# Kernel tuning notes

Hardware: AMD Instinct MI355X
Metric: run time of the kernel (lower is better)

## Reference

```python
import jax, jax.numpy as jnp
import numpy as np

LN_EPS = 1e-5
SM_EPS = 1e-16  # torch_geometric softmax denominator eps


def _layernorm(x, g, b):
    mu = jnp.mean(x, axis=-1, keepdims=True)
    var = jnp.var(x, axis=-1, keepdims=True)
    return (x - mu) * jax.lax.rsqrt(var + LN_EPS) * g + b


def setup_inputs() -> dict:
    d = 128
    L = 3
    N = 50000
    E = 800000
    key = jax.random.key(0)
    ks = jax.random.split(key, 16)
    s = 1.0 / np.sqrt(d)
    inp = {
        "edge_index": jax.random.randint(ks[0], (2, E), 0, N, dtype=jnp.int32),
        "x": jax.random.normal(ks[1], (N, d), dtype=jnp.float32),
        # per-layer attention params, stacked over layers
        "Wq": jax.random.uniform(ks[2], (L, d, d), jnp.float32, -s, s),
        "bq": jax.random.uniform(ks[3], (L, d), jnp.float32, -s, s),
        "Wk": jax.random.uniform(ks[4], (L, d, d), jnp.float32, -s, s),
        "bk": jax.random.uniform(ks[5], (L, d), jnp.float32, -s, s),
        "Wv": jax.random.uniform(ks[6], (L, d, d), jnp.float32, -s, s),
        "bv": jax.random.uniform(ks[7], (L, d), jnp.float32, -s, s),
        "ln_g": jnp.ones((L, d), jnp.float32),
        "ln_b": jnp.zeros((L, d), jnp.float32),
        # MLP stack: d -> 4d -> 2d -> d (no activations, per source)
        "W1": jax.random.uniform(ks[8], (4 * d, d), jnp.float32, -s, s),
        "b1": jax.random.uniform(ks[9], (4 * d,), jnp.float32, -s, s),
        "W2": jax.random.uniform(ks[10], (2 * d, 4 * d), jnp.float32, -0.5 * s, 0.5 * s),
        "b2": jax.random.uniform(ks[11], (2 * d,), jnp.float32, -0.5 * s, 0.5 * s),
        "W3": jax.random.uniform(ks[12], (d, 2 * d), jnp.float32, -0.7 * s, 0.7 * s),
        "b3": jax.random.uniform(ks[13], (d,), jnp.float32, -0.7 * s, 0.7 * s),
        "Wvec": jax.random.uniform(ks[14], (1, d), jnp.float32, -s, s),
        "bvec": jax.random.uniform(ks[15], (1,), jnp.float32, -s, s),
        "fn_g": jnp.ones((d,), jnp.float32),
        "fn_b": jnp.zeros((d,), jnp.float32),
    }
    return inp


def reference(edge_index, x, Wq, bq, Wk, bk, Wv, bv, ln_g, ln_b,
              W1, b1, W2, b2, W3, b3, Wvec, bvec, fn_g, fn_b):
    N = x.shape[0]
    src = edge_index[0]
    dst = edge_index[1]
    x_i = x[src]  # [E, d]
    x_j = x[dst]  # [E, d]
    L = Wq.shape[0]
    attn_output = None
    query = None
    for i in range(L):
        q = x_i @ Wq[i].T + bq[i]
        k = x_j @ Wk[i].T + bk[i]
        v = x_j @ Wv[i].T + bv[i]
        alpha = jnp.sum(q * k, axis=-1)  # [E]
        # segment softmax over destination node (torch_geometric.utils.softmax)
        m = jax.ops.segment_max(alpha, dst, num_segments=N)
        e = jnp.exp(alpha - m[dst])
        s = jax.ops.segment_sum(e, dst, num_segments=N)
        alpha = e / (s[dst] + SM_EPS)
        attn_output = jax.nn.relu(alpha[:, None] * v)  # dropout = identity (eval)
        query = _layernorm(x_j + attn_output, ln_g[i], ln_b[i])
    adj = attn_output  # squeeze(0) is a no-op for [E, d]
    adj = adj @ W1.T + b1
    adj = adj @ W2.T + b2
    adj = adj @ W3.T + b3
    adj = _layernorm(adj + query, fn_g, fn_b)
    adj_logits = (adj @ Wvec.T + bvec)[:, 0]  # [E]
    return adj_logits
```

## Files before the change

### kernel.cpp

```cpp
#include <hip/hip_runtime.h>


typedef __attribute__((ext_vector_type(8))) short bf16x8;
typedef __attribute__((ext_vector_type(4))) float f32x4;

__device__ __forceinline__ unsigned short f2bf(float f) {
  unsigned int u = __float_as_uint(f);
  unsigned int r = (u + 0x7fffu + ((u >> 16) & 1u)) >> 16;
  return (unsigned short)r;
}
__device__ __forceinline__ float blo(unsigned int u) {
  return __uint_as_float(u << 16);
}
__device__ __forceinline__ float bhi(unsigned int u) {
  return __uint_as_float(u & 0xffff0000u);
}

__global__ __launch_bounds__(128) void k_TW(
    const float* __restrict__ W2, const float* __restrict__ W1,
    const float* __restrict__ Wq, const float* __restrict__ Wk,
    const float* __restrict__ Wv, float* __restrict__ T,
    unsigned short* __restrict__ Wqb, unsigned short* __restrict__ Wkb,
    unsigned short* __restrict__ Wvb, float* __restrict__ sArr, int N) {
  const int b = blockIdx.x, t = threadIdx.x;
  if (b < 256) {
    float acc = 0.f;
    for (int k = 0; k < 512; ++k) acc += W2[b * 512 + k] * W1[k * 128 + t];
    T[b * 128 + t] = acc;
  } else if (b < 640) {
    const int idx = (b - 256) * 128 + t;
    const int m = idx >> 14, i = idx & 16383;
    const float* s = (m == 0) ? Wq : (m == 1) ? Wk : Wv;
    unsigned short* d = (m == 0) ? Wqb : (m == 1) ? Wkb : Wvb;
    d[i] = f2bf(s[i]);
  } else {
    const int i = (b - 640) * 128 + t;
    if (i < N) sArr[i] = 0.f;
  }
}

__global__ __launch_bounds__(256) void k_Ac(
    const float* __restrict__ W3, const float* __restrict__ T,
    const float* __restrict__ W2, const float* __restrict__ b1,
    const float* __restrict__ b2, const float* __restrict__ b3,
    const float* __restrict__ g, const float* __restrict__ lb,
    const float* __restrict__ fg, const float* __restrict__ fb,
    const float* __restrict__ wv, unsigned short* __restrict__ A3b,
    float* __restrict__ cfull, float* __restrict__ C) {
  __shared__ float t1[256];
  __shared__ float cf[128];
  const int b = blockIdx.x, t = threadIdx.x;
  if (b < 64) {
    const int i = 2 * b + (t >> 7), j = t & 127;
    float acc = 0.f;
    for (int k = 0; k < 256; ++k) acc += W3[i * 256 + k] * T[k * 128 + j];
    A3b[i * 128 + j] = f2bf(acc);
    return;
  }
  float acc = b2[t];
  for (int c = 0; c < 512; ++c) acc += W2[t * 512 + c] * b1[c];
  t1[t] = acc;
  __syncthreads();
  if (t < 128) {
    float a = b3[t];
    for (int k = 0; k < 256; ++k) a += W3[t * 256 + k] * t1[k];
    cfull[t] = a;
    cf[t] = a;
  }
  __syncthreads();
  if (t < 64) {
    const int l = t;
    const float2 gv = ((const float2*)g)[l];
    const float2 bv = ((const float2*)lb)[l];
    const float2 fgv = ((const float2*)fg)[l];
    const float2 fbv = ((const float2*)fb)[l];
    const float2 wvv = ((const float2*)wv)[l];
    const float P0 = cf[2 * l] + bv.x, P1 = cf[2 * l + 1] + bv.y;
    const float w0 = fgv.x * wvv.x, w1 = fgv.y * wvv.y;
    float s[9];
    s[0] = P0 + P1;
    s[1] = P0 * w0 + P1 * w1;
    s[2] = P0 * P0 + P1 * P1;
    s[3] = gv.x + gv.y;
    s[4] = gv.x * w0 + gv.y * w1;
    s[5] = gv.x * gv.x + gv.y * gv.y;
    s[6] = P0 * gv.x + P1 * gv.y;
    s[7] = w0 + w1;
    s[8] = fbv.x * wvv.x + fbv.y * wvv.y;
#pragma unroll
    for (int m = 32; m >= 1; m >>= 1)
#pragma unroll
      for (int i = 0; i < 9; ++i) s[i] += __shfl_xor(s[i], m, 64);
    if (l == 0)
#pragma unroll
      for (int i = 0; i < 9; ++i) C[i] = s[i];
  }
}

__global__ __launch_bounds__(256) void k_node(
    const float* __restrict__ x, const unsigned short* __restrict__ Wqb,
    const unsigned short* __restrict__ Wkb,
    const unsigned short* __restrict__ Wvb,
    const unsigned short* __restrict__ A3b, const float* __restrict__ bq,
    const float* __restrict__ bk, const float* __restrict__ bv,
    const float* __restrict__ cfull, const float* __restrict__ g,
    const float* __restrict__ lb, const float* __restrict__ fg,
    const float* __restrict__ wvp, unsigned short* __restrict__ Qb,
    unsigned short* __restrict__ Kb, float* __restrict__ S, int N) {
  __shared__ unsigned short tile[64][136];
  __shared__ unsigned short wl[128 * 128];
  const int t = threadIdx.x;
  const int nb = blockIdx.x * 64;
  for (int i = t; i < 64 * 32; i += 256) {
    const int j = i >> 5, c4 = i & 31;
    const int n = nb + j;
    float4 v = make_float4(0.f, 0.f, 0.f, 0.f);
    if (n < N) v = ((const float4*)x)[(size_t)n * 32 + c4];
    unsigned int lo = f2bf(v.x) | ((unsigned int)f2bf(v.y) << 16);
    unsigned int hi = f2bf(v.z) | ((unsigned int)f2bf(v.w) << 16);
    *(uint2*)&tile[j][c4 << 2] = make_uint2(lo, hi);
  }
  __syncthreads();
  const int wv16 = __builtin_amdgcn_readfirstlane(t >> 6) * 16;
  const int l = t & 63;
  const int ln = l & 15, g4 = l >> 4;
  bf16x8 af[4];
#pragma unroll
  for (int kb = 0; kb < 4; ++kb)
    af[kb] = *(const bf16x8*)&tile[wv16 + ln][kb * 32 + g4 * 8];

#define STAGE_W(MAT)                                                          \
  {                                                                           \
    __syncthreads();           \
    _Pragma("unroll") for (int c = 0; c < 8; ++c) {                           \
      const int idx = c * 256 + t;                                            \
      const int byte = idx * 16;                                              \
      const int row = byte >> 8;                                              \
      const int swz = byte ^ ((row & 7) << 4);                                \
      *(uint4*)((char*)wl + swz) =                                            \
          *(const uint4*)((const char*)(MAT) + byte);                         \
    }                                                                         \
    __syncthreads();                                                          \
  }
#define WFRAG(CB, KB)                                                         \
  (*(const bf16x8*)((const char*)wl +                                         \
                    (((((CB)*16 + ln) << 8) + (KB)*64 + g4 * 16) ^            \
                     ((ln & 7) << 4))))

  STAGE_W(Wqb)
#pragma unroll
  for (int cb = 0; cb < 8; ++cb) {
    f32x4 acc = {0.f, 0.f, 0.f, 0.f};
#pragma unroll
    for (int kb = 0; kb < 4; ++kb)
      acc = __builtin_amdgcn_mfma_f32_16x16x32_bf16(af[kb], WFRAG(cb, kb),
                                                    acc, 0, 0, 0);
    const int col = cb * 16 + ln;
    const float bs = bq[col];
#pragma unroll
    for (int r = 0; r < 4; ++r) tile[wv16 + g4 * 4 + r][col] = f2bf(acc[r] + bs);
  }
#pragma unroll
  for (int c = 0; c < 4; ++c) {
    const int row = wv16 + c * 4 + g4;
    const int n = nb + row;
    if (n < N)
      ((uint4*)(Qb + (size_t)n * 128))[ln] = *(const uint4*)&tile[row][ln * 8];
  }

  STAGE_W(Wkb)
#pragma unroll
  for (int cb = 0; cb < 8; ++cb) {
    f32x4 acc = {0.f, 0.f, 0.f, 0.f};
#pragma unroll
    for (int kb = 0; kb < 4; ++kb)
      acc = __builtin_amdgcn_mfma_f32_16x16x32_bf16(af[kb], WFRAG(cb, kb),
                                                    acc, 0, 0, 0);
    const int col = cb * 16 + ln;
    const float bs = bk[col];
#pragma unroll
    for (int r = 0; r < 4; ++r) tile[wv16 + g4 * 4 + r][col] = f2bf(acc[r] + bs);
  }
#pragma unroll
  for (int c = 0; c < 4; ++c) {
    const int row = wv16 + c * 4 + g4;
    const int n = nb + row;
    if (n < N)
      ((uint4*)(Kb + (size_t)n * 128))[ln] = *(const uint4*)&tile[row][ln * 8];
  }

  STAGE_W(Wvb)
  float uf[8][4];
#pragma unroll
  for (int cb = 0; cb < 8; ++cb) {
    f32x4 acc = {0.f, 0.f, 0.f, 0.f};
#pragma unroll
    for (int kb = 0; kb < 4; ++kb)
      acc = __builtin_amdgcn_mfma_f32_16x16x32_bf16(af[kb], WFRAG(cb, kb),
                                                    acc, 0, 0, 0);
    const int col = cb * 16 + ln;
    const float bs = bv[col];
#pragma unroll
    for (int r = 0; r < 4; ++r) {
      const float v = fmaxf(acc[r] + bs, 0.f);
      uf[cb][r] = v;
      tile[wv16 + g4 * 4 + r][col] = f2bf(v);
    }
  }

  bf16x8 af2[4];
#pragma unroll
  for (int kb = 0; kb < 4; ++kb)
    af2[kb] = *(const bf16x8*)&tile[wv16 + ln][kb * 32 + g4 * 8];
  STAGE_W(A3b)
  float vmf[8][4];
#pragma unroll
  for (int cb = 0; cb < 8; ++cb) {
    f32x4 acc = {0.f, 0.f, 0.f, 0.f};
#pragma unroll
    for (int kb = 0; kb < 4; ++kb)
      acc = __builtin_amdgcn_mfma_f32_16x16x32_bf16(af2[kb], WFRAG(cb, kb),
                                                    acc, 0, 0, 0);
#pragma unroll
    for (int r = 0; r < 4; ++r) vmf[cb][r] = acc[r];
  }
#undef STAGE_W
#undef WFRAG

  float gc[8], wc[8], Pc[8];
#pragma unroll
  for (int cb = 0; cb < 8; ++cb) {
    const int col = cb * 16 + ln;
    gc[cb] = g[col];
    wc[cb] = fg[col] * wvp[col];
    Pc[cb] = cfull[col] + lb[col];
  }

#pragma unroll
  for (int r = 0; r < 4; ++r) {
    const int row = wv16 + g4 * 4 + r;
    const int nrow = (nb + row < N) ? (nb + row) : (N - 1);
    float s[23];
#pragma unroll
    for (int i = 0; i < 23; ++i) s[i] = 0.f;
#pragma unroll
    for (int cb = 0; cb < 8; ++cb) {
      const float xv = x[(size_t)nrow * 128 + cb * 16 + ln];
      const float u = uf[cb][r];
      const float v = vmf[cb][r];
      const float gg = gc[cb], ww = wc[cb], PP = Pc[cb];
      const float xg = xv * gg, ug = u * gg;
      s[0] += xv;
      s[1] += u;
      s[2] += xv * xv;
      s[3] += xv * u;
      s[4] += u * u;
      s[5] += v;
      s[6] += v * ww;
      s[7] += xg;
      s[8] += ug;
      s[9] += xg * ww;
      s[10] += ug * ww;
      s[11] += PP * v;
      s[12] += v * v;
      s[13] += PP * xg;
      s[14] += PP * ug;
      s[15] += v * xg;
      s[16] += v * ug;
      s[17] += v * gg;
      s[18] += xg * xg;
      s[19] += xg * ug;
      s[20] += ug * ug;
      s[21] += xg * gg;
      s[22] += ug * gg;
    }
#pragma unroll
    for (int m = 1; m <= 8; m <<= 1)
#pragma unroll
      for (int i = 0; i < 23; ++i) s[i] += __shfl_xor(s[i], m, 64);
    const int n2 = nb + row;
    if (ln == 0 && n2 < N) {
      float* o = S + (size_t)n2 * 24;
      o[0] = s[0] * (1.f / 128.f);
      o[1] = s[1] * (1.f / 128.f);
#pragma unroll
      for (int i = 2; i < 23; ++i) o[i] = s[i];
      o[23] = 0.f;
    }
  }
}

__global__ __launch_bounds__(256) void k_edge_alpha(
    const int* __restrict__ ei, const unsigned short* __restrict__ Qb,
    const unsigned short* __restrict__ Kb, float* __restrict__ eArr,
    float* __restrict__ sArr, int E) {
  const int t = threadIdx.x;
  const int l = t & 15;
  const int e = blockIdx.x * 16 + (t >> 4);
  if (e >= E) return;
  const int src = ei[e];
  const int dst = ei[E + e];
  const uint4 qv = ((const uint4*)Qb)[(size_t)src * 16 + l];
  const uint4 kv = ((const uint4*)Kb)[(size_t)dst * 16 + l];
  float p = blo(qv.x) * blo(kv.x);
  p = fmaf(bhi(qv.x), bhi(kv.x), p);
  p = fmaf(blo(qv.y), blo(kv.y), p);
  p = fmaf(bhi(qv.y), bhi(kv.y), p);
  p = fmaf(blo(qv.z), blo(kv.z), p);
  p = fmaf(bhi(qv.z), bhi(kv.z), p);
  p = fmaf(blo(qv.w), blo(kv.w), p);
  p = fmaf(bhi(qv.w), bhi(kv.w), p);
#pragma unroll
  for (int m = 8; m >= 1; m >>= 1) p += __shfl_xor(p, m, 16);
  if (l == 0) {
    const float ex = __expf(p);
    eArr[e] = ex;
    atomicAdd(&sArr[dst], ex);
  }
}

__global__ __launch_bounds__(256) void k_edge_out(
    const int* __restrict__ ei, const float* __restrict__ eArr,
    const float* __restrict__ sArr, const float* __restrict__ S,
    const float* __restrict__ C, const float* __restrict__ bvec,
    float* __restrict__ out, int E) {
  const int e = blockIdx.x * 256 + threadIdx.x;
  if (e >= E) return;
  const int dst = ei[E + e];
  const float t = eArr[e] / (sArr[dst] + 1e-16f);
  const float4* o = (const float4*)(S + (size_t)dst * 24);
  const float4 q0 = o[0], q1 = o[1], q2 = o[2], q3 = o[3], q4 = o[4],
               q5 = o[5];
  const float mx = q0.x, mU = q0.y, sxx = q0.z, sxu = q0.w;
  const float suu = q1.x, sv = q1.y, svw = q1.z, sxg = q1.w;
  const float sug = q2.x, sxgw = q2.y, sugw = q2.z, spv = q2.w;
  const float svv = q3.x, pxg = q3.y, pug = q3.z, vxg = q3.w;
  const float vug = q4.x, vg = q4.y, xgxg = q4.z, xgug = q4.w;
  const float ugug = q5.x, xgg = q5.y, ugg = q5.z;
  const float SP = C[0], SPw = C[1], SPP = C[2], SG = C[3], SGw = C[4],
              GG = C[5], SPG = C[6], Sw = C[7], s0 = C[8];
  const float mu = mx + t * mU;
  const float qy = (sxx + 2.f * t * sxu + t * t * suu) * (1.f / 128.f);
  const float i1 = rsqrtf(qy - mu * mu + 1e-5f);
  const float sz = SP + t * sv + i1 * (sxg + t * sug - mu * SG);
  const float szw = SPw + t * svw + i1 * (sxgw + t * sugw - mu * SGw);
  const float cross = pxg + t * (pug + vxg) + t * t * vug - mu * (SPG + t * vg);
  const float rr = xgxg + 2.f * t * xgug + t * t * ugug -
                   2.f * mu * (xgg + t * ugg) + mu * mu * GG;
  const float szz =
      SPP + 2.f * t * spv + t * t * svv + 2.f * i1 * cross + i1 * i1 * rr;
  const float muz = sz * (1.f / 128.f);
  const float varz = szz * (1.f / 128.f) - muz * muz;
  const float iz = rsqrtf(varz + 1e-5f);
  out[e] = iz * (szw - muz * Sw) + s0 + bvec[0];
}

extern "C" void kernel_launch(void* const* d_in, const int* in_sizes, int n_in,
                              void* d_out, int out_size, void* d_ws,
                              size_t ws_size, hipStream_t stream) {
  const int* ei = (const int*)d_in[0];
  const float* x = (const float*)d_in[1];
  const float* Wq = (const float*)d_in[2];
  const float* bq = (const float*)d_in[3];
  const float* Wk = (const float*)d_in[4];
  const float* bk = (const float*)d_in[5];
  const float* Wv = (const float*)d_in[6];
  const float* bv = (const float*)d_in[7];
  const float* ln_g = (const float*)d_in[8];
  const float* ln_b = (const float*)d_in[9];
  const float* W1 = (const float*)d_in[10];
  const float* b1 = (const float*)d_in[11];
  const float* W2 = (const float*)d_in[12];
  const float* b2 = (const float*)d_in[13];
  const float* W3 = (const float*)d_in[14];
  const float* b3 = (const float*)d_in[15];
  const float* Wvec = (const float*)d_in[16];
  const float* bvec = (const float*)d_in[17];
  const float* fn_g = (const float*)d_in[18];
  const float* fn_b = (const float*)d_in[19];

  const int E = in_sizes[0] / 2;
  const int N = in_sizes[1] / 128;

  const float* Wq2 = Wq + 2 * 128 * 128;
  const float* bq2 = bq + 2 * 128;
  const float* Wk2 = Wk + 2 * 128 * 128;
  const float* bk2 = bk + 2 * 128;
  const float* Wv2 = Wv + 2 * 128 * 128;
  const float* bv2 = bv + 2 * 128;
  const float* g2 = ln_g + 2 * 128;
  const float* lb2 = ln_b + 2 * 128;

  float* ws = (float*)d_ws;
  float* T = ws;
  float* cfull = T + 32768;
  float* consts = cfull + 128;
  unsigned short* Wqb = (unsigned short*)(consts + 16);
  unsigned short* Wkb = Wqb + 16384;
  unsigned short* Wvb = Wkb + 16384;
  unsigned short* A3b = Wvb + 16384;
  float* fbase = consts + 16 + 32768;
  unsigned short* Qb = (unsigned short*)fbase;
  unsigned short* Kb = Qb + (size_t)N * 128;
  float* S = fbase + (size_t)N * 128;
  float* eArr = S + (size_t)N * 24;
  float* sArr = eArr + E;

  const int zblk = (N + 127) / 128;
  k_TW<<<640 + zblk, 128, 0, stream>>>(W2, W1, Wq2, Wk2, Wv2, T, Wqb, Wkb,
                                       Wvb, sArr, N);
  k_Ac<<<65, 256, 0, stream>>>(W3, T, W2, b1, b2, b3, g2, lb2, fn_g, fn_b,
                               Wvec, A3b, cfull, consts);

  const int nblk = (N + 63) / 64;
  k_node<<<nblk, 256, 0, stream>>>(x, Wqb, Wkb, Wvb, A3b, bq2, bk2, bv2,
                                   cfull, g2, lb2, fn_g, Wvec, Qb, Kb, S, N);
  const int ablk = (E + 15) / 16;
  k_edge_alpha<<<ablk, 256, 0, stream>>>(ei, Qb, Kb, eArr, sArr, E);
  const int oblk = (E + 255) / 256;
  k_edge_out<<<oblk, 256, 0, stream>>>(ei, eArr, sArr, S, consts, bvec,
                                       (float*)d_out, E);
}
```

Before: 181.4 us.

## Counting-sort edges by destination for locality in edge kernels

```diff
diff --git a/kernel.cpp b/kernel.cpp
--- a/kernel.cpp
+++ b/kernel.cpp
@@ -21,7 +21,7 @@
     const float* __restrict__ Wq, const float* __restrict__ Wk,
     const float* __restrict__ Wv, float* __restrict__ T,
     unsigned short* __restrict__ Wqb, unsigned short* __restrict__ Wkb,
-    unsigned short* __restrict__ Wvb, float* __restrict__ sArr, int N) {
+    unsigned short* __restrict__ Wvb, float* __restrict__ zbase, int NZ) {
   const int b = blockIdx.x, t = threadIdx.x;
   if (b < 256) {
     float acc = 0.f;
@@ -35,7 +35,7 @@
     d[i] = f2bf(s[i]);
   } else {
     const int i = (b - 640) * 128 + t;
-    if (i < N) sArr[i] = 0.f;
+    if (i < NZ) zbase[i] = 0.f;
   }
 }
 
@@ -95,6 +95,63 @@
 #pragma unroll
       for (int i = 0; i < 9; ++i) C[i] = s[i];
   }
+}
+
+__global__ __launch_bounds__(256) void k_hist(const int* __restrict__ ei,
+                                              int* __restrict__ hist, int E) {
+  const int e = blockIdx.x * 256 + threadIdx.x;
+  if (e < E) atomicAdd(&hist[ei[E + e]], 1);
+}
+
+__global__ __launch_bounds__(1024) void k_scan(const int* __restrict__ hist,
+                                               int* __restrict__ offsets,
+                                               int* __restrict__ cursor,
+                                               int N) {
+  __shared__ int wsum[16];
+  const int t = threadIdx.x;
+  const int chunk = (N + 1023) / 1024;
+  const int lo = t * chunk;
+  const int hi = (lo + chunk < N) ? lo + chunk : N;
+  int s = 0;
+  for (int i = lo; i < hi; ++i) s += hist[i];
+  int inc = s;
+#pragma unroll
+  for (int d = 1; d < 64; d <<= 1) {
+    const int up = __shfl_up(inc, d, 64);
+    if ((t & 63) >= d) inc += up;
+  }
+  if ((t & 63) == 63) wsum[t >> 6] = inc;
+  __syncthreads();
+  if (t < 16) {
+    const int v = wsum[t];
+    int inc2 = v;
+#pragma unroll
+    for (int d = 1; d < 16; d <<= 1) {
+      const int up = __shfl_up(inc2, d, 16);
+      if (t >= d) inc2 += up;
+    }
+    wsum[t] = inc2 - v;
+  }
+  __syncthreads();
+  int run = wsum[t >> 6] + (inc - s);
+  for (int i = lo; i < hi; ++i) {
+    offsets[i] = run;
+    cursor[i] = run;
+    run += hist[i];
+  }
+}
+
+__global__ __launch_bounds__(256) void k_scatter(
+    const int* __restrict__ ei, int* __restrict__ cursor,
+    int* __restrict__ sortedSrc, int* __restrict__ sortedDst,
+    int* __restrict__ origIdx, int E) {
+  const int e = blockIdx.x * 256 + threadIdx.x;
+  if (e >= E) return;
+  const int dst = ei[E + e];
+  const int pos = atomicAdd(&cursor[dst], 1);
+  sortedSrc[pos] = ei[e];
+  sortedDst[pos] = dst;
+  origIdx[pos] = e;
 }
 
 __global__ __launch_bounds__(256) void k_node(
@@ -131,7 +188,7 @@
 
 #define STAGE_W(MAT)                                                          \
   {                                                                           \
-    __syncthreads();           \
+    __syncthreads();                                                          \
     _Pragma("unroll") for (int c = 0; c < 8; ++c) {                           \
       const int idx = c * 256 + t;                                            \
       const int byte = idx * 16;                                              \
@@ -290,16 +347,17 @@
   }
 }
 
-__global__ __launch_bounds__(256) void k_edge_alpha(
-    const int* __restrict__ ei, const unsigned short* __restrict__ Qb,
-    const unsigned short* __restrict__ Kb, float* __restrict__ eArr,
+__global__ __launch_bounds__(256) void k_edge_alpha_s(
+    const int* __restrict__ sortedSrc, const int* __restrict__ sortedDst,
+    const unsigned short* __restrict__ Qb,
+    const unsigned short* __restrict__ Kb, float* __restrict__ eS,
     float* __restrict__ sArr, int E) {
   const int t = threadIdx.x;
   const int l = t & 15;
   const int e = blockIdx.x * 16 + (t >> 4);
   if (e >= E) return;
-  const int src = ei[e];
-  const int dst = ei[E + e];
+  const int src = sortedSrc[e];
+  const int dst = sortedDst[e];
   const uint4 qv = ((const uint4*)Qb)[(size_t)src * 16 + l];
   const uint4 kv = ((const uint4*)Kb)[(size_t)dst * 16 + l];
   float p = blo(qv.x) * blo(kv.x);
@@ -314,20 +372,20 @@
   for (int m = 8; m >= 1; m >>= 1) p += __shfl_xor(p, m, 16);
   if (l == 0) {
     const float ex = __expf(p);
-    eArr[e] = ex;
+    eS[e] = ex;
     atomicAdd(&sArr[dst], ex);
   }
 }
 
-__global__ __launch_bounds__(256) void k_edge_out(
-    const int* __restrict__ ei, const float* __restrict__ eArr,
-    const float* __restrict__ sArr, const float* __restrict__ S,
-    const float* __restrict__ C, const float* __restrict__ bvec,
-    float* __restrict__ out, int E) {
+__global__ __launch_bounds__(256) void k_edge_out_s(
+    const int* __restrict__ sortedDst, const int* __restrict__ origIdx,
+    const float* __restrict__ eS, const float* __restrict__ sArr,
+    const float* __restrict__ S, const float* __restrict__ C,
+    const float* __restrict__ bvec, float* __restrict__ out, int E) {
   const int e = blockIdx.x * 256 + threadIdx.x;
   if (e >= E) return;
-  const int dst = ei[E + e];
-  const float t = eArr[e] / (sArr[dst] + 1e-16f);
+  const int dst = sortedDst[e];
+  const float t = eS[e] / (sArr[dst] + 1e-16f);
   const float4* o = (const float4*)(S + (size_t)dst * 24);
   const float4 q0 = o[0], q1 = o[1], q2 = o[2], q3 = o[3], q4 = o[4],
                q5 = o[5];
@@ -352,7 +410,7 @@
   const float muz = sz * (1.f / 128.f);
   const float varz = szz * (1.f / 128.f) - muz * muz;
   const float iz = rsqrtf(varz + 1e-5f);
-  out[e] = iz * (szw - muz * Sw) + s0 + bvec[0];
+  out[origIdx[e]] = iz * (szw - muz * Sw) + s0 + bvec[0];
 }
 
 extern "C" void kernel_launch(void* const* d_in, const int* in_sizes, int n_in,
@@ -403,21 +461,32 @@
   unsigned short* Qb = (unsigned short*)fbase;
   unsigned short* Kb = Qb + (size_t)N * 128;
   float* S = fbase + (size_t)N * 128;
-  float* eArr = S + (size_t)N * 24;
-  float* sArr = eArr + E;
-
-  const int zblk = (N + 127) / 128;
+  float* eS = S + (size_t)N * 24;
+  float* sArr = eS + E;
+  int* hist = (int*)(sArr + N);
+  int* offsets = hist + N;
+  int* cursor = offsets + N;
+  int* sortedSrc = cursor + N;
+  int* sortedDst = sortedSrc + E;
+  int* origIdx = sortedDst + E;
+
+  const int zblk = (2 * N + 127) / 128;
   k_TW<<<640 + zblk, 128, 0, stream>>>(W2, W1, Wq2, Wk2, Wv2, T, Wqb, Wkb,
-                                       Wvb, sArr, N);
+                                       Wvb, sArr, 2 * N);
+  const int eblk256 = (E + 255) / 256;
+  k_hist<<<eblk256, 256, 0, stream>>>(ei, hist, E);
   k_Ac<<<65, 256, 0, stream>>>(W3, T, W2, b1, b2, b3, g2, lb2, fn_g, fn_b,
                                Wvec, A3b, cfull, consts);
+  k_scan<<<1, 1024, 0, stream>>>(hist, offsets, cursor, N);
+  k_scatter<<<eblk256, 256, 0, stream>>>(ei, cursor, sortedSrc, sortedDst,
+                                         origIdx, E);
 
   const int nblk = (N + 63) / 64;
   k_node<<<nblk, 256, 0, stream>>>(x, Wqb, Wkb, Wvb, A3b, bq2, bk2, bv2,
                                    cfull, g2, lb2, fn_g, Wvec, Qb, Kb, S, N);
   const int ablk = (E + 15) / 16;
-  k_edge_alpha<<<ablk, 256, 0, stream>>>(ei, Qb, Kb, eArr, sArr, E);
-  const int oblk = (E + 255) / 256;
-  k_edge_out<<<oblk, 256, 0, stream>>>(ei, eArr, sArr, S, consts, bvec,
-                                       (float*)d_out, E);
-}
+  k_edge_alpha_s<<<ablk, 256, 0, stream>>>(sortedSrc, sortedDst, Qb, Kb, eS,
+                                           sArr, E);
+  k_edge_out_s<<<eblk256, 256, 0, stream>>>(sortedDst, origIdx, eS, sArr, S,
+                                            consts, bvec, (float*)d_out, E);
+}
```

Measured after the change: 363.3 us. +100.3%, slower.

## Double-buffer weight staging in halves to overlap loads with MFMA

Applied to the files above, without the earlier changes.

```diff
diff --git a/kernel.cpp b/kernel.cpp
--- a/kernel.cpp
+++ b/kernel.cpp
@@ -108,7 +108,7 @@
     const float* __restrict__ wvp, unsigned short* __restrict__ Qb,
     unsigned short* __restrict__ Kb, float* __restrict__ S, int N) {
   __shared__ unsigned short tile[64][136];
-  __shared__ unsigned short wl[128 * 128];
+  __shared__ unsigned short wl[2][64 * 128];
   const int t = threadIdx.x;
   const int nb = blockIdx.x * 64;
   for (int i = t; i < 64 * 32; i += 256) {
@@ -129,103 +129,107 @@
   for (int kb = 0; kb < 4; ++kb)
     af[kb] = *(const bf16x8*)&tile[wv16 + ln][kb * 32 + g4 * 8];
 
-#define STAGE_W(MAT)                                                          \
+#define STAGE_HALF(MAT, HALF, BUF)                                            \
   {                                                                           \
-    __syncthreads();           \
-    _Pragma("unroll") for (int c = 0; c < 8; ++c) {                           \
+    _Pragma("unroll") for (int c = 0; c < 4; ++c) {                           \
       const int idx = c * 256 + t;                                            \
       const int byte = idx * 16;                                              \
-      const int row = byte >> 8;                                              \
-      const int swz = byte ^ ((row & 7) << 4);                                \
-      *(uint4*)((char*)wl + swz) =                                            \
-          *(const uint4*)((const char*)(MAT) + byte);                         \
+      const int lrow = byte >> 8;                                             \
+      const int swz = byte ^ ((lrow & 7) << 4);                               \
+      *(uint4*)((char*)wl[BUF] + swz) =                                       \
+          *(const uint4*)((const char*)(MAT) + (HALF)*16384 + byte);          \
     }                                                                         \
-    __syncthreads();                                                          \
-  }
-#define WFRAG(CB, KB)                                                         \
-  (*(const bf16x8*)((const char*)wl +                                         \
-                    (((((CB)*16 + ln) << 8) + (KB)*64 + g4 * 16) ^            \
+  }
+#define WFRAG2(BUF, CBL, KB)                                                  \
+  (*(const bf16x8*)((const char*)wl[BUF] +                                    \
+                    (((((CBL)*16 + ln) << 8) + (KB)*64 + g4 * 16) ^           \
                      ((ln & 7) << 4))))
 
-  STAGE_W(Wqb)
-#pragma unroll
-  for (int cb = 0; cb < 8; ++cb) {
-    f32x4 acc = {0.f, 0.f, 0.f, 0.f};
-#pragma unroll
-    for (int kb = 0; kb < 4; ++kb)
-      acc = __builtin_amdgcn_mfma_f32_16x16x32_bf16(af[kb], WFRAG(cb, kb),
-                                                    acc, 0, 0, 0);
-    const int col = cb * 16 + ln;
-    const float bs = bq[col];
-#pragma unroll
-    for (int r = 0; r < 4; ++r) tile[wv16 + g4 * 4 + r][col] = f2bf(acc[r] + bs);
-  }
-#pragma unroll
-  for (int c = 0; c < 4; ++c) {
-    const int row = wv16 + c * 4 + g4;
-    const int n = nb + row;
-    if (n < N)
-      ((uint4*)(Qb + (size_t)n * 128))[ln] = *(const uint4*)&tile[row][ln * 8];
-  }
-
-  STAGE_W(Wkb)
-#pragma unroll
-  for (int cb = 0; cb < 8; ++cb) {
-    f32x4 acc = {0.f, 0.f, 0.f, 0.f};
-#pragma unroll
-    for (int kb = 0; kb < 4; ++kb)
-      acc = __builtin_amdgcn_mfma_f32_16x16x32_bf16(af[kb], WFRAG(cb, kb),
-                                                    acc, 0, 0, 0);
-    const int col = cb * 16 + ln;
-    const float bs = bk[col];
-#pragma unroll
-    for (int r = 0; r < 4; ++r) tile[wv16 + g4 * 4 + r][col] = f2bf(acc[r] + bs);
-  }
-#pragma unroll
-  for (int c = 0; c < 4; ++c) {
-    const int row = wv16 + c * 4 + g4;
-    const int n = nb + row;
-    if (n < N)
-      ((uint4*)(Kb + (size_t)n * 128))[ln] = *(const uint4*)&tile[row][ln * 8];
-  }
-
-  STAGE_W(Wvb)
+#define HALF_QKV(BUF, HALF, BIAS, RELU, UFSAVE)                               \
+  {                                                                           \
+    _Pragma("unroll") for (int cbl = 0; cbl < 4; ++cbl) {                     \
+      f32x4 acc = {0.f, 0.f, 0.f, 0.f};                                       \
+      _Pragma("unroll") for (int kb = 0; kb < 4; ++kb) acc =                  \
+          __builtin_amdgcn_mfma_f32_16x16x32_bf16(af[kb],                     \
+                                                  WFRAG2(BUF, cbl, kb), acc,  \
+                                                  0, 0, 0);                   \
+      const int col = ((HALF)*4 + cbl) * 16 + ln;                             \
+      const float bs = (BIAS)[col];                                           \
+      _Pragma("unroll") for (int r = 0; r < 4; ++r) {                         \
+        float v = acc[r] + bs;                                                \
+        if (RELU) v = fmaxf(v, 0.f);                                          \
+        if (UFSAVE) uf[(HALF)*4 + cbl][r] = v;                                \
+        tile[wv16 + g4 * 4 + r][col] = f2bf(v);                               \
+      }                                                                       \
+    }                                                                         \
+  }
+#define STORE_TILE(DST)                                                       \
+  {                                                                           \
+    _Pragma("unroll") for (int c = 0; c < 4; ++c) {                           \
+      const int row = wv16 + c * 4 + g4;                                      \
+      const int n = nb + row;                                                 \
+      if (n < N) ((uint4*)((DST) + (size_t)n * 128))[ln] =                    \
+          *(const uint4*)&tile[row][ln * 8];                                  \
+    }                                                                         \
+  }
+
   float uf[8][4];
-#pragma unroll
-  for (int cb = 0; cb < 8; ++cb) {
-    f32x4 acc = {0.f, 0.f, 0.f, 0.f};
-#pragma unroll
-    for (int kb = 0; kb < 4; ++kb)
-      acc = __builtin_amdgcn_mfma_f32_16x16x32_bf16(af[kb], WFRAG(cb, kb),
-                                                    acc, 0, 0, 0);
-    const int col = cb * 16 + ln;
-    const float bs = bv[col];
-#pragma unroll
-    for (int r = 0; r < 4; ++r) {
-      const float v = fmaxf(acc[r] + bs, 0.f);
-      uf[cb][r] = v;
-      tile[wv16 + g4 * 4 + r][col] = f2bf(v);
-    }
-  }
-
+
+  STAGE_HALF(Wqb, 0, 0)
+  __syncthreads();
+  STAGE_HALF(Wqb, 1, 1)
+  HALF_QKV(0, 0, bq, false, false)
+  __syncthreads();
+  STAGE_HALF(Wkb, 0, 0)
+  HALF_QKV(1, 1, bq, false, false)
+  STORE_TILE(Qb)
+  __syncthreads();
+  STAGE_HALF(Wkb, 1, 1)
+  HALF_QKV(0, 0, bk, false, false)
+  __syncthreads();
+  STAGE_HALF(Wvb, 0, 0)
+  HALF_QKV(1, 1, bk, false, false)
+  STORE_TILE(Kb)
+  __syncthreads();
+  STAGE_HALF(Wvb, 1, 1)
+  HALF_QKV(0, 0, bv, true, true)
+  __syncthreads();
+  STAGE_HALF(A3b, 0, 0)
+  HALF_QKV(1, 1, bv, true, true)
+  __syncthreads();
+  STAGE_HALF(A3b, 1, 1)
   bf16x8 af2[4];
 #pragma unroll
   for (int kb = 0; kb < 4; ++kb)
     af2[kb] = *(const bf16x8*)&tile[wv16 + ln][kb * 32 + g4 * 8];
-  STAGE_W(A3b)
   float vmf[8][4];
 #pragma unroll
-  for (int cb = 0; cb < 8; ++cb) {
+  for (int cbl = 0; cbl < 4; ++cbl) {
     f32x4 acc = {0.f, 0.f, 0.f, 0.f};
 #pragma unroll
     for (int kb = 0; kb < 4; ++kb)
-      acc = __builtin_amdgcn_mfma_f32_16x16x32_bf16(af2[kb], WFRAG(cb, kb),
-                                                    acc, 0, 0, 0);
-#pragma unroll
-    for (int r = 0; r < 4; ++r) vmf[cb][r] = acc[r];
-  }
-#undef STAGE_W
-#undef WFRAG
+      acc = __builtin_amdgcn_mfma_f32_16x16x32_bf16(af2[kb],
+                                                    WFRAG2(0, cbl, kb), acc,
+                                                    0, 0, 0);
+#pragma unroll
+    for (int r = 0; r < 4; ++r) vmf[cbl][r] = acc[r];
+  }
+  __syncthreads();
+#pragma unroll
+  for (int cbl = 0; cbl < 4; ++cbl) {
+    f32x4 acc = {0.f, 0.f, 0.f, 0.f};
+#pragma unroll
+    for (int kb = 0; kb < 4; ++kb)
+      acc = __builtin_amdgcn_mfma_f32_16x16x32_bf16(af2[kb],
+                                                    WFRAG2(1, cbl, kb), acc,
+                                                    0, 0, 0);
+#pragma unroll
+    for (int r = 0; r < 4; ++r) vmf[4 + cbl][r] = acc[r];
+  }
+#undef STAGE_HALF
+#undef WFRAG2
+#undef HALF_QKV
+#undef STORE_TILE
 
   float gc[8], wc[8], Pc[8];
 #pragma unroll
```

Result: no change. 182.0 us (+0.4%).
